# Performance work log

Measured on AMD Instinct MI355X. Metric: run time of the kernel, lower is better.

## Reference

```python
import jax, jax.numpy as jnp
import numpy as np

MEDNUM = 50000
FEATDIM = 128
NNZ = 3200000
N = 2 * MEDNUM  # adjacency is over cat([mEmbed, mEmbed])


def setup_inputs() -> dict:
    key = jax.random.key(0)
    k1, k2, k3, k4, k5 = jax.random.split(key, 5)
    vals = jax.random.uniform(k1, (NNZ,), dtype=jnp.float32)
    mEmbed = jax.random.normal(k2, (MEDNUM, FEATDIM), dtype=jnp.float32)
    inter = jax.random.normal(k3, (1,), dtype=jnp.float32)
    row_idx = jax.random.randint(k4, (NNZ,), 0, N, dtype=jnp.int32)
    col_idx = jax.random.randint(k5, (NNZ,), 0, N, dtype=jnp.int32)
    return {"vals": vals, "mEmbed": mEmbed, "inter": inter,
            "row_idx": row_idx, "col_idx": col_idx}


def _gcn_layer(vals, row_idx, col_idx, embeds):
    # spmm(adj, embeds) via gather + weighted segment-sum, then LeakyReLU(0.5)
    gathered = embeds[col_idx] * vals[:, None]          # [E, F]
    agg = jax.ops.segment_sum(gathered, row_idx, num_segments=N)  # [N, F]
    return jnp.where(agg >= 0, agg, 0.5 * agg)          # LeakyReLU(negative_slope=0.5)


def reference(vals, mEmbed, inter, row_idx, col_idx):
    embeds1 = jnp.concatenate([mEmbed, mEmbed], axis=0)  # [2*mednum, F]
    # Source quirk: lats1 is never extended, so both iterations use embeds1.
    tem1 = jax.nn.relu(_gcn_layer(vals, row_idx, col_idx, embeds1))
    gnnEmbeds1 = tem1 + tem1                              # sum of two identical layers
    m1 = gnnEmbeds1[:MEDNUM]
    m2 = gnnEmbeds1[MEDNUM:]
    return inter * m1 + (1.0 - inter) * m2
```

## Files before the change

kernel.cpp:

```cpp
#include <hip/hip_runtime.h>

#define MEDNUM 50000
#define FEATDIM 128
#define NNZ 3200000
#define NBUCK 1563
#define SLAB 2304
#define PART_BLOCKS 250
#define PART_E 12800
#define PART_K 25
#define CAP SLAB

#define OFF_CUR    0
#define OFF_SCALE  1600
#define OFF_QT     51600
#define OFF_RECS   3251600


__global__ __launch_bounds__(256) void toint8_kernel(const float* __restrict__ mEmbed,
                                                     unsigned short* __restrict__ qt,
                                                     float* __restrict__ scales,
                                                     int* __restrict__ gcur) {
    int g = blockIdx.x * 256 + threadIdx.x;
    if (g < NBUCK) gcur[g] = g * SLAB;

    int row = blockIdx.x * 4 + (threadIdx.x >> 6);
    int lane = threadIdx.x & 63;
    if (row >= MEDNUM) return;
    float2 f = ((const float2*)(mEmbed + (long long)row * FEATDIM))[lane];
    float m = fmaxf(fabsf(f.x), fabsf(f.y));
    for (int o = 32; o > 0; o >>= 1) m = fmaxf(m, __shfl_xor(m, o, 64));
    float inv = (m > 0.f) ? 127.f / m : 0.f;
    float s   = (m > 0.f) ? m / 127.f : 0.f;
    int q0 = __float2int_rn(f.x * inv) + 128;
    int q1 = __float2int_rn(f.y * inv) + 128;
    qt[(long long)row * 64 + ((lane & 15) * 4 + (lane >> 4))] =
        (unsigned short)((q0 & 0xff) | ((q1 & 0xff) << 8));
    if (lane == 0) scales[row] = s;
}

__global__ __launch_bounds__(512, 2) void part_kernel(const float* __restrict__ vals,
                                                      const int* __restrict__ row_idx,
                                                      const int* __restrict__ col_idx,
                                                      const float* __restrict__ scales,
                                                      int* __restrict__ gcur,
                                                      unsigned long long* __restrict__ recs) {
    __shared__ unsigned long long lrec[PART_E];
    __shared__ int lcnt[NBUCK];
    __shared__ int gstart[NBUCK];
    __shared__ int wsum[8];

    int tid = threadIdx.x;
    int base = blockIdx.x * PART_E;

    for (int i = tid; i < NBUCK; i += 512) lcnt[i] = 0;
    __syncthreads();

    unsigned long long rec[PART_K];
    {
        int rr[PART_K], cc[PART_K];
        float vv[PART_K];
#pragma unroll
        for (int k = 0; k < PART_K; k++) {
            int e = base + k * 512 + tid;
            rr[k] = __builtin_nontemporal_load(row_idx + e);
            cc[k] = __builtin_nontemporal_load(col_idx + e);
            vv[k] = __builtin_nontemporal_load(vals + e);
        }
        float ss[PART_K];
#pragma unroll
        for (int k = 0; k < PART_K; k++) {
            cc[k] = (cc[k] >= MEDNUM) ? cc[k] - MEDNUM : cc[k];
            ss[k] = scales[cc[k]];
        }
#pragma unroll
        for (int k = 0; k < PART_K; k++) {
            int r = rr[k], half = 0;
            if (r >= MEDNUM) { r -= MEDNUM; half = 1; }
            float vp = vv[k] * ss[k];
            int b = r >> 5;
            int rib = (r & 31) | (half << 5);
            rec[k] = ((unsigned long long)__float_as_uint(vp) << 32)
                   | ((unsigned long long)(b >> 10) << 63)
                   | ((unsigned int)(b & 0x3FF) << 22)
                   | ((unsigned int)rib << 16)
                   | (unsigned int)cc[k];
            atomicAdd(&lcnt[b], 1);
        }
    }
    __syncthreads();

    int i0 = tid * 4;
    int c0 = 0, c1 = 0, c2 = 0, c3 = 0;
    if (i0 < NBUCK)     c0 = lcnt[i0];
    if (i0 + 1 < NBUCK) c1 = lcnt[i0 + 1];
    if (i0 + 2 < NBUCK) c2 = lcnt[i0 + 2];
    if (i0 + 3 < NBUCK) c3 = lcnt[i0 + 3];
    int s = c0 + c1 + c2 + c3;
    int x = s;
#pragma unroll
    for (int d = 1; d < 64; d <<= 1) {
        int t = __shfl_up(x, d, 64);
        if ((tid & 63) >= d) x += t;
    }
    int wave = tid >> 6, lane = tid & 63;
    if (lane == 63) wsum[wave] = x;
    __syncthreads();
    if (tid == 0) {
        int acc = 0;
#pragma unroll
        for (int w = 0; w < 8; w++) { int t = wsum[w]; wsum[w] = acc; acc += t; }
    }
    __syncthreads();
    int excl = wsum[wave] + x - s;

    {
        int e = excl;
        int cs[4] = {c0, c1, c2, c3};
#pragma unroll
        for (int q = 0; q < 4; q++) {
            int i = i0 + q;
            if (i < NBUCK) {
                int c = cs[q];
                if (c > 0) {
                    int gb = atomicAdd(&gcur[i], c);
                    gstart[i] = gb - e;
                }
                lcnt[i] = e;
                e += c;
            }
        }
    }
    __syncthreads();

#pragma unroll
    for (int k = 0; k < PART_K; k++) {
        unsigned long long r = rec[k];
        int b = (int)(((r >> 53) & 0x400u) | ((r >> 22) & 0x3FFu));
        int pos = atomicAdd(&lcnt[b], 1);
        lrec[pos] = r;
    }
    __syncthreads();

#pragma unroll
    for (int k = 0; k < PART_K; k++) {
        int j = k * 512 + tid;
        unsigned long long r = lrec[j];
        int b = (int)(((r >> 53) & 0x400u) | ((r >> 22) & 0x3FFu));
        int addr = gstart[b] + j;
        recs[addr] = r & 0x7FFFFFFFFFFFFFFFULL;
    }
}

__device__ __forceinline__ void accum4_body(const unsigned int p[4],
                                            const unsigned short* __restrict__ qt,
                                            unsigned int flo,
                                            float acc[8], float& sv) {
    unsigned long long w[4];
#pragma unroll
    for (int q = 0; q < 4; q++)
        w[q] = *(const unsigned long long*)((const char*)qt
                   + (((p[q] & 0xffffu) << 7) | flo));
#pragma unroll
    for (int q = 0; q < 4; q++) {
        float v = __uint_as_float(p[q] & 0xffff0000u);
        sv += v;
        unsigned int wlo = (unsigned int)w[q], whi = (unsigned int)(w[q] >> 32);
        acc[0] = fmaf(v, (float)(wlo & 0xffu),         acc[0]);
        acc[1] = fmaf(v, (float)((wlo >> 8) & 0xffu),  acc[1]);
        acc[2] = fmaf(v, (float)((wlo >> 16) & 0xffu), acc[2]);
        acc[3] = fmaf(v, (float)(wlo >> 24),           acc[3]);
        acc[4] = fmaf(v, (float)(whi & 0xffu),         acc[4]);
        acc[5] = fmaf(v, (float)((whi >> 8) & 0xffu),  acc[5]);
        acc[6] = fmaf(v, (float)((whi >> 16) & 0xffu), acc[6]);
        acc[7] = fmaf(v, (float)(whi >> 24),           acc[7]);
    }
}

__device__ __forceinline__ void seg_to_pair(int s, int e,
                                            const unsigned int* __restrict__ st4,
                                            const unsigned short* __restrict__ qt,
                                            int qw, unsigned int flo,
                                            float& rx, float& ry) {
    float acc[8], sv;
#pragma unroll
    for (int x = 0; x < 8; x++) acc[x] = 0.f;
    sv = 0.f;
    int i = s;
    for (; i + 16 <= e; i += 16) {
        unsigned int p[4];
#pragma unroll
        for (int q = 0; q < 4; q++) p[q] = st4[i + q * 4 + qw];
        accum4_body(p, qt, flo, acc, sv);
    }
    if (i < e) {
        unsigned int p[4];
#pragma unroll
        for (int q = 0; q < 4; q++) {
            int j = i + q * 4 + qw;
            p[q] = (j < e) ? st4[j] : 0u;
        }
        accum4_body(p, qt, flo, acc, sv);
    }
#pragma unroll
    for (int x = 0; x < 8; x++) {
        acc[x] += __shfl_xor(acc[x], 16, 64);
        acc[x] += __shfl_xor(acc[x], 32, 64);
    }
    sv += __shfl_xor(sv, 16, 64);
    sv += __shfl_xor(sv, 32, 64);
    float sx = (qw & 2) ? ((qw & 1) ? acc[6] : acc[4]) : ((qw & 1) ? acc[2] : acc[0]);
    float sy = (qw & 2) ? ((qw & 1) ? acc[7] : acc[5]) : ((qw & 1) ? acc[3] : acc[1]);
    rx = fmaxf(fmaf(-128.f, sv, sx), 0.f);
    ry = fmaxf(fmaf(-128.f, sv, sy), 0.f);
}

__global__ __launch_bounds__(512, 6) void agg_kernel(const int* __restrict__ gcur,
                                                     const unsigned long long* __restrict__ recs,
                                                     const unsigned short* __restrict__ qt,
                                                     const float* __restrict__ inter,
                                                     float* __restrict__ out) {
    __shared__ unsigned long long slab8[CAP];
    __shared__ unsigned int st4[CAP];
    __shared__ int cnt[64];
    __shared__ int bas[65];
    int b = blockIdx.x, tid = threadIdx.x;
    long long gs = (long long)b * SLAB;
    int n = gcur[b] - b * SLAB;
    if (n > CAP) n = CAP;

    if (tid < 64) cnt[tid] = 0;
    for (int j = tid; j < n; j += 512)
        slab8[j] = __builtin_nontemporal_load(recs + gs + j);
    __syncthreads();
    for (int j = tid; j < n; j += 512)
        atomicAdd(&cnt[(int)((slab8[j] >> 16) & 63)], 1);
    __syncthreads();
    if (tid < 64) {
        int v = cnt[tid];
        int x = v;
#pragma unroll
        for (int d = 1; d < 64; d <<= 1) {
            int tmp = __shfl_up(x, d, 64);
            if (tid >= d) x += tmp;
        }
        bas[tid] = x - v;
        if (tid == 63) bas[64] = x;
        cnt[tid] = x - v;
    }
    __syncthreads();
    for (int j = tid; j < n; j += 512) {
        unsigned long long r = slab8[j];
        int rib = (int)((r >> 16) & 63);
        int p = atomicAdd(&cnt[rib], 1);
        unsigned int vb = (unsigned int)(r >> 32);
        vb = (vb + 0x7fffu + ((vb >> 16) & 1u)) & 0xffff0000u;
        st4[p] = ((unsigned int)(r & 0xffff)) | vb;
    }
    __syncthreads();
    float t = inter[0];
    float s1 = 2.f * t, s2 = 2.f * (1.f - t);
    int wave = tid >> 6, lane = tid & 63;
    int qw = lane >> 4;
    unsigned int flo = (unsigned int)((lane & 15) << 3);
#pragma unroll 1
    for (int i2 = 0; i2 < 4; i2++) {
        int rib0 = wave * 4 + i2;
        int frow = b * 32 + rib0;
        if (frow >= MEDNUM) break;
        float ax, ay, cx, cy;
        seg_to_pair(bas[rib0],      bas[rib0 + 1],  st4, qt, qw, flo, ax, ay);
        seg_to_pair(bas[rib0 + 32], bas[rib0 + 33], st4, qt, qw, flo, cx, cy);
        float ox = s1 * ax + s2 * cx;
        float oy = s1 * ay + s2 * cy;
        unsigned long long packed =
            (unsigned long long)__float_as_uint(ox)
          | ((unsigned long long)__float_as_uint(oy) << 32);
        __builtin_nontemporal_store(packed,
            (unsigned long long*)(out + (long long)frow * FEATDIM + lane * 2));
    }
}

extern "C" void kernel_launch(void* const* d_in, const int* in_sizes, int n_in,
                              void* d_out, int out_size, void* d_ws, size_t ws_size,
                              hipStream_t stream) {
    const float* vals    = (const float*)d_in[0];
    const float* mEmbed  = (const float*)d_in[1];
    const float* inter   = (const float*)d_in[2];
    const int*   row_idx = (const int*)d_in[3];
    const int*   col_idx = (const int*)d_in[4];
    float* out = (float*)d_out;

    int* ws = (int*)d_ws;
    int* gcur = ws + OFF_CUR;
    float* scales = (float*)(ws + OFF_SCALE);
    unsigned short* qt = (unsigned short*)(ws + OFF_QT);
    unsigned long long* recs = (unsigned long long*)(ws + OFF_RECS);

    toint8_kernel<<<(MEDNUM + 3) / 4, 256, 0, stream>>>(mEmbed, qt, scales, gcur);
    part_kernel<<<PART_BLOCKS, 512, 0, stream>>>(vals, row_idx, col_idx, scales, gcur, recs);
    agg_kernel<<<NBUCK, 512, 0, stream>>>(gcur, recs, qt, inter, out);
}
```

Before: 220.9 us.

## Double partition block threads, widen aggregation gather batch, fuse slab load with histogram

The partition kernel now runs 1024 threads per block, so each thread handles 12 edges plus an optional tail, and the bucket scan covers 2 buckets per thread across 16 waves. The aggregation inner loop gathers 8 quantized rows per step instead of 4, giving more loads in flight. The slab load and the per-row histogram in the aggregation kernel are merged into one pass, removing a shared-memory reread. The risks are higher register pressure and the launch-bounds hint of 4 blocks of 1024 threads, which cannot be met given the large shared-memory footprint.

Result: faster. 198.2 us, median of 2 (-10.3%).

```diff
diff --git a/kernel.cpp b/kernel.cpp
--- a/kernel.cpp
+++ b/kernel.cpp
@@ -7,7 +7,9 @@
 #define SLAB 2304
 #define PART_BLOCKS 250
 #define PART_E 12800
-#define PART_K 25
+#define PART_T 1024
+#define PART_K 12
+#define PART_TAIL 512
 #define CAP SLAB
 
 #define OFF_CUR    0
@@ -38,39 +40,53 @@
     if (lane == 0) scales[row] = s;
 }
 
-__global__ __launch_bounds__(512, 2) void part_kernel(const float* __restrict__ vals,
-                                                      const int* __restrict__ row_idx,
-                                                      const int* __restrict__ col_idx,
-                                                      const float* __restrict__ scales,
-                                                      int* __restrict__ gcur,
-                                                      unsigned long long* __restrict__ recs) {
+__global__ __launch_bounds__(PART_T, 4) void part_kernel(const float* __restrict__ vals,
+                                                         const int* __restrict__ row_idx,
+                                                         const int* __restrict__ col_idx,
+                                                         const float* __restrict__ scales,
+                                                         int* __restrict__ gcur,
+                                                         unsigned long long* __restrict__ recs) {
     __shared__ unsigned long long lrec[PART_E];
     __shared__ int lcnt[NBUCK];
     __shared__ int gstart[NBUCK];
-    __shared__ int wsum[8];
+    __shared__ int wsum[16];
 
     int tid = threadIdx.x;
     int base = blockIdx.x * PART_E;
 
-    for (int i = tid; i < NBUCK; i += 512) lcnt[i] = 0;
+    for (int i = tid; i < NBUCK; i += PART_T) lcnt[i] = 0;
     __syncthreads();
 
     unsigned long long rec[PART_K];
+    unsigned long long rtail = 0;
+    int have_tail = (tid < PART_TAIL);
     {
         int rr[PART_K], cc[PART_K];
         float vv[PART_K];
 #pragma unroll
         for (int k = 0; k < PART_K; k++) {
-            int e = base + k * 512 + tid;
+            int e = base + k * PART_T + tid;
             rr[k] = __builtin_nontemporal_load(row_idx + e);
             cc[k] = __builtin_nontemporal_load(col_idx + e);
             vv[k] = __builtin_nontemporal_load(vals + e);
         }
+        int rt = 0, ct = 0; float vt = 0.f;
+        if (have_tail) {
+            int e = base + PART_K * PART_T + tid;
+            rt = __builtin_nontemporal_load(row_idx + e);
+            ct = __builtin_nontemporal_load(col_idx + e);
+            vt = __builtin_nontemporal_load(vals + e);
+        }
         float ss[PART_K];
 #pragma unroll
         for (int k = 0; k < PART_K; k++) {
             cc[k] = (cc[k] >= MEDNUM) ? cc[k] - MEDNUM : cc[k];
             ss[k] = scales[cc[k]];
+        }
+        float st = 0.f;
+        if (have_tail) {
+            ct = (ct >= MEDNUM) ? ct - MEDNUM : ct;
+            st = scales[ct];
         }
 #pragma unroll
         for (int k = 0; k < PART_K; k++) {
@@ -86,16 +102,27 @@
                    | (unsigned int)cc[k];
             atomicAdd(&lcnt[b], 1);
         }
-    }
-    __syncthreads();
-
-    int i0 = tid * 4;
-    int c0 = 0, c1 = 0, c2 = 0, c3 = 0;
+        if (have_tail) {
+            int r = rt, half = 0;
+            if (r >= MEDNUM) { r -= MEDNUM; half = 1; }
+            float vp = vt * st;
+            int b = r >> 5;
+            int rib = (r & 31) | (half << 5);
+            rtail = ((unsigned long long)__float_as_uint(vp) << 32)
+                  | ((unsigned long long)(b >> 10) << 63)
+                  | ((unsigned int)(b & 0x3FF) << 22)
+                  | ((unsigned int)rib << 16)
+                  | (unsigned int)ct;
+            atomicAdd(&lcnt[b], 1);
+        }
+    }
+    __syncthreads();
+
+    int i0 = tid * 2;
+    int c0 = 0, c1 = 0;
     if (i0 < NBUCK)     c0 = lcnt[i0];
     if (i0 + 1 < NBUCK) c1 = lcnt[i0 + 1];
-    if (i0 + 2 < NBUCK) c2 = lcnt[i0 + 2];
-    if (i0 + 3 < NBUCK) c3 = lcnt[i0 + 3];
-    int s = c0 + c1 + c2 + c3;
+    int s = c0 + c1;
     int x = s;
 #pragma unroll
     for (int d = 1; d < 64; d <<= 1) {
@@ -108,26 +135,22 @@
     if (tid == 0) {
         int acc = 0;
 #pragma unroll
-        for (int w = 0; w < 8; w++) { int t = wsum[w]; wsum[w] = acc; acc += t; }
+        for (int w = 0; w < 16; w++) { int t = wsum[w]; wsum[w] = acc; acc += t; }
     }
     __syncthreads();
     int excl = wsum[wave] + x - s;
 
     {
         int e = excl;
-        int cs[4] = {c0, c1, c2, c3};
-#pragma unroll
-        for (int q = 0; q < 4; q++) {
-            int i = i0 + q;
-            if (i < NBUCK) {
-                int c = cs[q];
-                if (c > 0) {
-                    int gb = atomicAdd(&gcur[i], c);
-                    gstart[i] = gb - e;
-                }
-                lcnt[i] = e;
-                e += c;
-            }
+        if (i0 < NBUCK) {
+            if (c0 > 0) gstart[i0] = atomicAdd(&gcur[i0], c0) - e;
+            lcnt[i0] = e;
+            e += c0;
+        }
+        if (i0 + 1 < NBUCK) {
+            if (c1 > 0) gstart[i0 + 1] = atomicAdd(&gcur[i0 + 1], c1) - e;
+            lcnt[i0 + 1] = e;
+            e += c1;
         }
     }
     __syncthreads();
@@ -139,29 +162,40 @@
         int pos = atomicAdd(&lcnt[b], 1);
         lrec[pos] = r;
     }
+    if (have_tail) {
+        unsigned long long r = rtail;
+        int b = (int)(((r >> 53) & 0x400u) | ((r >> 22) & 0x3FFu));
+        int pos = atomicAdd(&lcnt[b], 1);
+        lrec[pos] = r;
+    }
     __syncthreads();
 
 #pragma unroll
     for (int k = 0; k < PART_K; k++) {
-        int j = k * 512 + tid;
+        int j = k * PART_T + tid;
         unsigned long long r = lrec[j];
         int b = (int)(((r >> 53) & 0x400u) | ((r >> 22) & 0x3FFu));
-        int addr = gstart[b] + j;
-        recs[addr] = r & 0x7FFFFFFFFFFFFFFFULL;
-    }
-}
-
-__device__ __forceinline__ void accum4_body(const unsigned int p[4],
+        recs[gstart[b] + j] = r & 0x7FFFFFFFFFFFFFFFULL;
+    }
+    if (have_tail) {
+        int j = PART_K * PART_T + tid;
+        unsigned long long r = lrec[j];
+        int b = (int)(((r >> 53) & 0x400u) | ((r >> 22) & 0x3FFu));
+        recs[gstart[b] + j] = r & 0x7FFFFFFFFFFFFFFFULL;
+    }
+}
+
+__device__ __forceinline__ void accum8_body(const unsigned int p[8],
                                             const unsigned short* __restrict__ qt,
                                             unsigned int flo,
                                             float acc[8], float& sv) {
-    unsigned long long w[4];
-#pragma unroll
-    for (int q = 0; q < 4; q++)
+    unsigned long long w[8];
+#pragma unroll
+    for (int q = 0; q < 8; q++)
         w[q] = *(const unsigned long long*)((const char*)qt
                    + (((p[q] & 0xffffu) << 7) | flo));
 #pragma unroll
-    for (int q = 0; q < 4; q++) {
+    for (int q = 0; q < 8; q++) {
         float v = __uint_as_float(p[q] & 0xffff0000u);
         sv += v;
         unsigned int wlo = (unsigned int)w[q], whi = (unsigned int)(w[q] >> 32);
@@ -186,20 +220,20 @@
     for (int x = 0; x < 8; x++) acc[x] = 0.f;
     sv = 0.f;
     int i = s;
-    for (; i + 16 <= e; i += 16) {
-        unsigned int p[4];
-#pragma unroll
-        for (int q = 0; q < 4; q++) p[q] = st4[i + q * 4 + qw];
-        accum4_body(p, qt, flo, acc, sv);
+    for (; i + 32 <= e; i += 32) {
+        unsigned int p[8];
+#pragma unroll
+        for (int q = 0; q < 8; q++) p[q] = st4[i + q * 4 + qw];
+        accum8_body(p, qt, flo, acc, sv);
     }
     if (i < e) {
-        unsigned int p[4];
-#pragma unroll
-        for (int q = 0; q < 4; q++) {
+        unsigned int p[8];
+#pragma unroll
+        for (int q = 0; q < 8; q++) {
             int j = i + q * 4 + qw;
             p[q] = (j < e) ? st4[j] : 0u;
         }
-        accum4_body(p, qt, flo, acc, sv);
+        accum8_body(p, qt, flo, acc, sv);
     }
 #pragma unroll
     for (int x = 0; x < 8; x++) {
@@ -229,11 +263,12 @@
     if (n > CAP) n = CAP;
 
     if (tid < 64) cnt[tid] = 0;
-    for (int j = tid; j < n; j += 512)
-        slab8[j] = __builtin_nontemporal_load(recs + gs + j);
-    __syncthreads();
-    for (int j = tid; j < n; j += 512)
-        atomicAdd(&cnt[(int)((slab8[j] >> 16) & 63)], 1);
+    __syncthreads();
+    for (int j = tid; j < n; j += 512) {
+        unsigned long long r = __builtin_nontemporal_load(recs + gs + j);
+        slab8[j] = r;
+        atomicAdd(&cnt[(int)((r >> 16) & 63)], 1);
+    }
     __syncthreads();
     if (tid < 64) {
         int v = cnt[tid];
@@ -297,6 +332,6 @@
     unsigned long long* recs = (unsigned long long*)(ws + OFF_RECS);
 
     toint8_kernel<<<(MEDNUM + 3) / 4, 256, 0, stream>>>(mEmbed, qt, scales, gcur);
-    part_kernel<<<PART_BLOCKS, 512, 0, stream>>>(vals, row_idx, col_idx, scales, gcur, recs);
+    part_kernel<<<PART_BLOCKS, PART_T, 0, stream>>>(vals, row_idx, col_idx, scales, gcur, recs);
     agg_kernel<<<NBUCK, 512, 0, stream>>>(gcur, recs, qt, inter, out);
 }
```
